# Optimization experiments

Hardware: AMD Instinct MI355X
Metric: run time of the kernel (lower is better)

Reference implementation:

```python
import jax, jax.numpy as jnp
import numpy as np

EPS = 1e-6
HEADS = 8


def _block_weights(gh, gw):
    # block centers at (i+0.5, j+0.5); 'cos' transform, column-normalized (sum over dim 0)
    ii, jj = np.meshgrid(np.arange(gh) + 0.5, np.arange(gw) + 0.5, indexing='ij')
    centers = np.stack([ii.ravel(), jj.ravel()], axis=-1)  # [N, 2]
    d = np.linalg.norm(centers[:, None, :] - centers[None, :, :], axis=-1)  # [N, N]
    mat = np.cos(d / d.max() * np.pi / 4.0)
    mat = mat / mat.sum(axis=0, keepdims=True)
    return jnp.asarray(mat, dtype=jnp.float32)


def setup_inputs() -> dict:
    key = jax.random.key(0)
    ks = jax.random.split(key, 5)
    B, N, W, C = 8, 256, 49, 512
    s = 1.0 / np.sqrt(C)
    return {
        'x': jax.random.normal(ks[0], (B, N, W, C), jnp.float32),
        'ln_g': jnp.ones((C,), jnp.float32),
        'ln_b': jnp.zeros((C,), jnp.float32),
        'w_qkv': jax.random.normal(ks[1], (3 * C, C), jnp.float32) * s,  # Linear(dim, 3*dim, bias=False)
        'lepe_w': jax.random.normal(ks[2], (C, 1, 5, 5), jnp.float32) * 0.2,  # depthwise 5x5
        'lepe_b': jnp.zeros((C,), jnp.float32),
        'w_out': jax.random.normal(ks[3], (C, C), jnp.float32) * s,
        'b_out': jnp.zeros((C,), jnp.float32),
    }


def reference(x, ln_g, ln_b, w_qkv, lepe_w, lepe_b, w_out, b_out):
    B, N, Wn, C = x.shape
    H = HEADS
    D = C // H
    gh = gw = int(round(N ** 0.5))   # grid of window blocks
    wh = ww = int(round(Wn ** 0.5))  # tokens per window side

    # LayerNorm over channel dim (torch eps=1e-5, biased var)
    mu = x.mean(-1, keepdims=True)
    var = x.var(-1, keepdims=True)
    xn = (x - mu) / jnp.sqrt(var + 1e-5) * ln_g + ln_b

    # qkv projection
    qkv = jnp.einsum('bnwc,oc->bnwo', xn, w_qkv)
    q, k, v = jnp.split(qkv, 3, axis=-1)  # each [B, N, W, C]

    # LePE: fold v to image [B, C, gh*wh, gw*ww], depthwise conv 5x5 pad 2, unfold back
    img = v.reshape(B, gh, gw, wh, ww, C).transpose(0, 5, 1, 3, 2, 4).reshape(B, C, gh * wh, gw * ww)
    lepe = jax.lax.conv_general_dilated(
        img, lepe_w, window_strides=(1, 1), padding=((2, 2), (2, 2)),
        dimension_numbers=('NCHW', 'OIHW', 'NCHW'), feature_group_count=C)
    lepe = lepe + lepe_b[None, :, None, None]
    lepe = lepe.reshape(B, C, gh, wh, gw, ww).transpose(0, 2, 4, 3, 5, 1).reshape(B, N, Wn, C)

    # ReLU + eps feature maps (qk_norm=False -> identity norms)
    q = jax.nn.relu(q) + EPS
    k = jax.nn.relu(k) + EPS

    # split heads: [B, H, N, W, D]
    def split_heads(t):
        return t.reshape(B, N, Wn, H, D).transpose(0, 3, 1, 2, 4)
    q, k, v = split_heads(q), split_heads(k), split_heads(v)

    # per-block k^T v state: [B, H, N, D, D]
    kv = jnp.einsum('bhnwd,bhnwe->bhnde', k, v)
    weight = _block_weights(gh, gw)  # [N, N]
    kv = jnp.einsum('ij,bhjde->bhide', weight, kv)

    k_sum = k.sum(axis=-2)  # [B, H, N, D]
    qk_sum = jnp.einsum('bhnwd,bhnd->bhnw', q, k_sum)[..., None]  # [B, H, N, W, 1]
    normalizer = jnp.einsum('ij,bhjwo->bhiwo', weight, qk_sum) + EPS

    out = jnp.einsum('bhnwd,bhnde->bhnwe', q, kv) / normalizer  # [B, H, N, W, D]
    out = out.transpose(0, 2, 3, 1, 4).reshape(B, N, Wn, C)
    out = out + lepe
    return jnp.einsum('bnwc,oc->bnwo', out, w_out) + b_out
```

## Files before the change

kernel.cpp:

```cpp
#include <hip/hip_runtime.h>
#include <cstdint>

typedef unsigned short u16;
typedef unsigned int   u32;
typedef u16   u16x8 __attribute__((ext_vector_type(8)));
typedef u16   u16x4 __attribute__((ext_vector_type(4)));
typedef float f32x4 __attribute__((ext_vector_type(4)));
typedef __bf16 bf16x8 __attribute__((ext_vector_type(8)));

#define NB    256
#define WTOK  49
#define CH    512
#define HEADS 8
#define DH    64
#define TOK   100352
#define CO    1536

__device__ __forceinline__ u16 f2bf(float f) {
  u32 u = __float_as_uint(f);
  u = (u + 0x7FFFu + ((u >> 16) & 1u)) >> 16;
  return (u16)u;
}
__device__ __forceinline__ float bf2f(u16 u) { return __uint_as_float(((u32)u) << 16); }

__device__ __forceinline__ void load_lds16(const void* g, void* l) {
  __builtin_amdgcn_global_load_lds(
      reinterpret_cast<__attribute__((address_space(1))) void*>(reinterpret_cast<uintptr_t>(g)),
      reinterpret_cast<__attribute__((address_space(3))) void*>(reinterpret_cast<uintptr_t>(l)),
      16, 0, 0);
}

__global__ void cvt_f32_bf16(const float* __restrict__ in, u16* __restrict__ out, int n8) {
  int i = blockIdx.x * 256 + threadIdx.x;
  if (i < n8) {
    f32x4 a = *(const f32x4*)(in + (long)i * 8);
    f32x4 b = *(const f32x4*)(in + (long)i * 8 + 4);
    u16x8 o;
    o[0]=f2bf(a[0]); o[1]=f2bf(a[1]); o[2]=f2bf(a[2]); o[3]=f2bf(a[3]);
    o[4]=f2bf(b[0]); o[5]=f2bf(b[1]); o[6]=f2bf(b[2]); o[7]=f2bf(b[3]);
    *(u16x8*)(out + (long)i * 8) = o;
  }
}

__global__ void prep_wle(const float* __restrict__ lepe_w, float* __restrict__ wle) {
  int i = blockIdx.x * 256 + threadIdx.x;
  if (i < 12800) {
    int c = i / 25, kk = i % 25;
    wle[kk * 512 + c] = lepe_w[i];
  }
}

__global__ void weight_kernel(u16* __restrict__ Wbf, float* __restrict__ Wt) {
  int j = blockIdx.x, i = threadIdx.x;
  float iy = (float)(i >> 4) + 0.5f, ix = (float)(i & 15) + 0.5f;
  float jy = (float)(j >> 4) + 0.5f, jx = (float)(j & 15) + 0.5f;
  float dy = iy - jy, dx = ix - jx;
  float d = sqrtf(dy * dy + dx * dx);
  const float dmax = 21.213203435596427f;
  float m = cosf(d * (0.78539816339744831f / dmax));
  __shared__ float red[256];
  red[i] = m;
  __syncthreads();
  for (int s = 128; s > 0; s >>= 1) {
    if (i < s) red[i] += red[i + s];
    __syncthreads();
  }
  float w = m / red[0];
  Wbf[i * 256 + j] = f2bf(w);
  Wt[j * 256 + i] = w;
}

__global__ __launch_bounds__(256) void ln_kernel(const float* __restrict__ x,
                                                 const float* __restrict__ g,
                                                 const float* __restrict__ bta,
                                                 u16* __restrict__ xn) {
  int wave = threadIdx.x >> 6, lane = threadIdx.x & 63;
  long t = (long)blockIdx.x * 4 + wave;
  const float* xp = x + t * CH + lane * 8;
  f32x4 a = *(const f32x4*)xp;
  f32x4 b = *(const f32x4*)(xp + 4);
  float s  = a[0]+a[1]+a[2]+a[3]+b[0]+b[1]+b[2]+b[3];
  float sq = a[0]*a[0]+a[1]*a[1]+a[2]*a[2]+a[3]*a[3]+b[0]*b[0]+b[1]*b[1]+b[2]*b[2]+b[3]*b[3];
  for (int m = 1; m < 64; m <<= 1) { s += __shfl_xor(s, m); sq += __shfl_xor(sq, m); }
  float mu = s * (1.0f / 512.0f);
  float var = sq * (1.0f / 512.0f) - mu * mu;
  float rstd = rsqrtf(var + 1e-5f);
  const float* gp = g + lane * 8;
  const float* bp = bta + lane * 8;
  f32x4 g0 = *(const f32x4*)gp, g1 = *(const f32x4*)(gp + 4);
  f32x4 b0 = *(const f32x4*)bp, b1 = *(const f32x4*)(bp + 4);
  u16x8 o;
  o[0] = f2bf((a[0]-mu)*rstd*g0[0] + b0[0]);
  o[1] = f2bf((a[1]-mu)*rstd*g0[1] + b0[1]);
  o[2] = f2bf((a[2]-mu)*rstd*g0[2] + b0[2]);
  o[3] = f2bf((a[3]-mu)*rstd*g0[3] + b0[3]);
  o[4] = f2bf((b[0]-mu)*rstd*g1[0] + b1[0]);
  o[5] = f2bf((b[1]-mu)*rstd*g1[1] + b1[1]);
  o[6] = f2bf((b[2]-mu)*rstd*g1[2] + b1[2]);
  o[7] = f2bf((b[3]-mu)*rstd*g1[3] + b1[3]);
  *(u16x8*)(xn + t * CH + lane * 8) = o;
}

template <int KT>
__device__ __forceinline__ void kstep8(char* sm, const u16* sA, const u16* sB,
                                       int t, int lane_off, int wm, int wn,
                                       f32x4 (&acc)[8][4]) {
  const char* base = sm + (KT & 3) * 32768 + lane_off;
  char* wbp = sm + ((KT + 3) & 3) * 32768 + t * 16;
  if constexpr (KT + 3 < 16) {
    load_lds16(sA + (KT + 3) * 32, wbp);
    load_lds16(sA + (KT + 3) * 32 + 65536, wbp + 8192);
  }
  bf16x8 bfr[4], afr[4];
#pragma unroll
  for (int n = 0; n < 4; n++) bfr[n] = *(const bf16x8*)(base + 16384 + wn * 4096 + n * 1024);
#pragma unroll
  for (int m = 0; m < 4; m++) afr[m] = *(const bf16x8*)(base + wm * 8192 + m * 1024);
  __builtin_amdgcn_s_barrier();
  __builtin_amdgcn_s_setprio(1);
#pragma unroll
  for (int m = 0; m < 4; m++)
#pragma unroll
    for (int n = 0; n < 4; n++)
      acc[m][n] = __builtin_amdgcn_mfma_f32_16x16x32_bf16(afr[m], bfr[n], acc[m][n], 0, 0, 0);
  __builtin_amdgcn_s_setprio(0);
  __builtin_amdgcn_s_barrier();
  if constexpr (KT + 3 < 16) {
    load_lds16(sB + (KT + 3) * 32, wbp + 16384);
    load_lds16(sB + (KT + 3) * 32 + 65536, wbp + 24576);
  }
#pragma unroll
  for (int m = 0; m < 4; m++) afr[m] = *(const bf16x8*)(base + wm * 8192 + (4 + m) * 1024);
  __builtin_amdgcn_s_barrier();
  __builtin_amdgcn_s_setprio(1);
#pragma unroll
  for (int m = 0; m < 4; m++)
#pragma unroll
    for (int n = 0; n < 4; n++)
      acc[4 + m][n] = __builtin_amdgcn_mfma_f32_16x16x32_bf16(afr[m], bfr[n], acc[4 + m][n], 0, 0, 0);
  __builtin_amdgcn_s_setprio(0);
  if constexpr (KT < 13) {
    asm volatile("s_waitcnt vmcnt(8)" ::: "memory");
  } else if constexpr (KT == 13) {
    asm volatile("s_waitcnt vmcnt(4)" ::: "memory");
  } else if constexpr (KT == 14) {
    asm volatile("s_waitcnt vmcnt(0)" ::: "memory");
  }
  if constexpr (KT < 15) __builtin_amdgcn_s_barrier();
}

template <int EPI>
__global__ __launch_bounds__(512, 2)
void gemm8(const u16* __restrict__ A, const u16* __restrict__ B,
           void* __restrict__ C, const float* __restrict__ bias, int N, int nbn) {
  __shared__ __align__(16) char sm[131072];
  const int nwg = gridDim.x;
  const int bid = blockIdx.x;
  const int cpx = nwg >> 3;
  const int vid = (bid & 7) * cpx + (bid >> 3);
  const int bn = vid % nbn, bm = vid / nbn;
  const int t = threadIdx.x;
  const int lane = t & 63, wave = t >> 6;
  const int wm = wave >> 2, wn = wave & 3;
  const int fr = lane & 15, fq = lane >> 4;
  const int lane_off = (fr >> 1) * 128 + ((((fr & 1) << 2) + fq) ^ (fr >> 1)) * 16;
  const int sl = (t & 7) ^ ((t >> 3) & 7);
  const u16* sA = A + ((long)bm * 256 + ((t >> 3) << 1) + (sl >> 2)) * 512 + (sl & 3) * 8;
  const u16* sB = B + ((long)bn * 256 + ((t >> 3) << 1) + (sl >> 2)) * 512 + (sl & 3) * 8;
  f32x4 acc[8][4] = {};
#pragma unroll
  for (int kt = 0; kt < 3; kt++) {
    char* d = sm + kt * 32768 + t * 16;
    load_lds16(sA + kt * 32, d);
    load_lds16(sA + kt * 32 + 65536, d + 8192);
    load_lds16(sB + kt * 32, d + 16384);
    load_lds16(sB + kt * 32 + 65536, d + 24576);
  }
  asm volatile("s_waitcnt vmcnt(8)" ::: "memory");
  __builtin_amdgcn_s_barrier();
  kstep8<0>(sm, sA, sB, t, lane_off, wm, wn, acc);
  kstep8<1>(sm, sA, sB, t, lane_off, wm, wn, acc);
  kstep8<2>(sm, sA, sB, t, lane_off, wm, wn, acc);
  kstep8<3>(sm, sA, sB, t, lane_off, wm, wn, acc);
  kstep8<4>(sm, sA, sB, t, lane_off, wm, wn, acc);
  kstep8<5>(sm, sA, sB, t, lane_off, wm, wn, acc);
  kstep8<6>(sm, sA, sB, t, lane_off, wm, wn, acc);
  kstep8<7>(sm, sA, sB, t, lane_off, wm, wn, acc);
  kstep8<8>(sm, sA, sB, t, lane_off, wm, wn, acc);
  kstep8<9>(sm, sA, sB, t, lane_off, wm, wn, acc);
  kstep8<10>(sm, sA, sB, t, lane_off, wm, wn, acc);
  kstep8<11>(sm, sA, sB, t, lane_off, wm, wn, acc);
  kstep8<12>(sm, sA, sB, t, lane_off, wm, wn, acc);
  kstep8<13>(sm, sA, sB, t, lane_off, wm, wn, acc);
  kstep8<14>(sm, sA, sB, t, lane_off, wm, wn, acc);
  kstep8<15>(sm, sA, sB, t, lane_off, wm, wn, acc);
  const long r0 = (long)bm * 256 + wm * 128 + fq * 4;
  const int c0 = bn * 256 + wn * 64 + fr;
#pragma unroll
  for (int m = 0; m < 8; m++) {
#pragma unroll
    for (int n = 0; n < 4; n++) {
      int c = c0 + n * 16;
#pragma unroll
      for (int jj = 0; jj < 4; jj++) {
        long r = r0 + m * 16 + jj;
        float v = acc[m][n][jj];
        if (EPI == 1) {
          if (c < 1024) v = fmaxf(v, 0.0f) + 1e-6f;
          ((u16*)C)[r * N + c] = f2bf(v);
        } else if (EPI == 2) {
          ((float*)C)[r * N + c] = v + bias[c];
        } else {
          ((u16*)C)[r * N + c] = f2bf(v);
        }
      }
    }
  }
}

template <int EPI>
__global__ __launch_bounds__(256)
void gemm_bt(const u16* __restrict__ A, const u16* __restrict__ B,
             void* __restrict__ C, const float* __restrict__ bias,
             int M, int N, int K, long sAb, long sBb, long sCb) {
  __shared__ u16 As[128 * 32];
  __shared__ u16 Bs[128 * 32];
  const int tid = threadIdx.x;
  const int lane = tid & 63;
  const int wave = tid >> 6;
  const int fr = lane & 15, fq = lane >> 4;
  const int wr = (wave >> 1) * 64, wc = (wave & 1) * 64;
  const long bm = blockIdx.y, bn = blockIdx.x, bz = blockIdx.z;
  const u16* Ab = A + bz * sAb + bm * 128 * (long)K;
  const u16* Bb = B + bz * sBb + bn * 128 * (long)K;
  const int srow = tid >> 2;
  const int scol = (tid & 3) * 8;
  f32x4 acc[4][4] = {};
  for (int k0 = 0; k0 < K; k0 += 32) {
    load_lds16(Ab + (long)srow * K + k0 + scol, As + tid * 8);
    load_lds16(Ab + (long)(srow + 64) * K + k0 + scol, As + 2048 + tid * 8);
    load_lds16(Bb + (long)srow * K + k0 + scol, Bs + tid * 8);
    load_lds16(Bb + (long)(srow + 64) * K + k0 + scol, Bs + 2048 + tid * 8);
    __syncthreads();
    bf16x8 af[4], bf[4];
#pragma unroll
    for (int m = 0; m < 4; m++) af[m] = *(const bf16x8*)&As[(wr + m * 16 + fr) * 32 + fq * 8];
#pragma unroll
    for (int n = 0; n < 4; n++) bf[n] = *(const bf16x8*)&Bs[(wc + n * 16 + fr) * 32 + fq * 8];
#pragma unroll
    for (int m = 0; m < 4; m++)
#pragma unroll
      for (int n = 0; n < 4; n++)
        acc[m][n] = __builtin_amdgcn_mfma_f32_16x16x32_bf16(af[m], bf[n], acc[m][n], 0, 0, 0);
    __syncthreads();
  }
#pragma unroll
  for (int m = 0; m < 4; m++) {
    int r0 = wr + m * 16 + fq * 4;
#pragma unroll
    for (int n = 0; n < 4; n++) {
      int c = (int)bn * 128 + wc + n * 16 + fr;
#pragma unroll
      for (int jj = 0; jj < 4; jj++) {
        long r = bm * 128 + r0 + jj;
        float v = acc[m][n][jj];
        if (EPI == 1) { if (c < 1024) v = fmaxf(v, 0.0f) + 1e-6f; }
        if (EPI == 2) {
          ((float*)C)[bz * sCb + r * N + c] = v + bias[c];
        } else {
          ((u16*)C)[bz * sCb + r * N + c] = f2bf(v);
        }
      }
    }
  }
}

__global__ __launch_bounds__(256)
void fold_v(const u16* __restrict__ qkv, u16* __restrict__ vimg) {
  long i = (long)blockIdx.x * 256 + threadIdx.x;
  int tok = (int)(i >> 6);
  int c0 = ((int)i & 63) * 8;
  int w = tok % WTOK, n = tok / WTOK;
  int b = n >> 8, blk = n & 255;
  int gi = blk >> 4, gj = blk & 15;
  int wi = w / 7, wj = w - wi * 7;
  int y = gi * 7 + wi + 2, x = gj * 7 + wj + 2;
  u16x8 v = *(const u16x8*)(qkv + (long)tok * CO + 1024 + c0);
  *(u16x8*)(vimg + (((long)(b * 116 + y)) * 116 + x) * 512 + c0) = v;
}

__global__ __launch_bounds__(256)
void zero_border(u16* __restrict__ vimg) {
  int y = blockIdx.x, b = blockIdx.y;
  int tid = threadIdx.x;
  u16* row = vimg + ((long)(b * 116 + y)) * 116 * 512;
  u16x8 z = {};
  if (y < 2 || y >= 114) {
    for (int i = tid; i < 116 * 512 / 8; i += 256) *(u16x8*)(row + i * 8) = z;
  } else {
    int col = tid >> 6;
    int x = (col < 2) ? col : 112 + col;
    *(u16x8*)(row + x * 512 + (tid & 63) * 8) = z;
  }
}

__global__ __launch_bounds__(256, 2)
void lepe_conv3(const u16* __restrict__ vimg, const float* __restrict__ wle,
                const float* __restrict__ lb, u16* __restrict__ lepe) {
  const int tid = threadIdx.x;
  const int c0 = (tid & 127) * 4;
  const int x  = blockIdx.x * 2 + (tid >> 7);
  const int ys = blockIdx.y * 14;
  const int b  = blockIdx.z;
  f32x4 wv[25];
#pragma unroll
  for (int k = 0; k < 25; k++) wv[k] = *(const f32x4*)(wle + k * 512 + c0);
  const f32x4 bias = *(const f32x4*)(lb + c0);
  const u16* rbase = vimg + (((long)(b * 116 + ys)) * 116 + x) * 512 + c0;
  u16x4 win[5][5];
#pragma unroll
  for (int j = 0; j < 4; j++) {
    const u16* rp = rbase + (long)j * (116 * 512);
#pragma unroll
    for (int kx = 0; kx < 5; kx++) win[j][kx] = *(const u16x4*)(rp + kx * 512);
  }
  const int gj = x / 7, wj = x - gj * 7;
  u16* ob = lepe + (((long)(b * 256 + blockIdx.y * 32 + gj)) * 49 + wj) * 512 + c0;
#pragma unroll
  for (int i = 0; i < 14; i++) {
    {
      const u16* rp = rbase + (long)(i + 4) * (116 * 512);
#pragma unroll
      for (int kx = 0; kx < 5; kx++) win[(i + 4) % 5][kx] = *(const u16x4*)(rp + kx * 512);
    }
    f32x4 acc = bias;
#pragma unroll
    for (int s = 0; s < 5; s++)
#pragma unroll
      for (int kx = 0; kx < 5; kx++) {
        u16x4 v = win[(i + s) % 5][kx];
        f32x4 w = wv[s * 5 + kx];
#pragma unroll
        for (int c = 0; c < 4; c++) acc[c] += bf2f(v[c]) * w[c];
      }
    u16x4 o;
#pragma unroll
    for (int c = 0; c < 4; c++) o[c] = f2bf(acc[c]);
    *(u16x4*)(ob + ((i / 7) * 784 + (i % 7) * 7) * 512) = o;
  }
}

__global__ __launch_bounds__(256)
void kv_local_kernel(const u16* __restrict__ qkv, u16* __restrict__ KVl,
                     float* __restrict__ qk_sum) {
  int n = blockIdx.x, h = blockIdx.y, b = blockIdx.z;
  int bh = b * HEADS + h;
  long tbase = ((long)(b * NB + n)) * WTOK;
  __shared__ u16 kT[64 * 72];
  __shared__ u16 vT[64 * 72];
  __shared__ u16 qs[49 * 72];
  __shared__ float ksum[64];
  __shared__ float qkp[256];
  int tid = threadIdx.x;
  for (int i = tid; i < (64 * 72) / 2; i += 256) {
    ((u32*)kT)[i] = 0;
    ((u32*)vT)[i] = 0;
  }
  __syncthreads();
  {
    int w = tid >> 3, d0 = (tid & 7) * 8;
    u16x8 k8 = *(const u16x8*)(qkv + (tbase + w) * CO + 512 + h * 64 + d0);
    u16x8 v8 = *(const u16x8*)(qkv + (tbase + w) * CO + 1024 + h * 64 + d0);
#pragma unroll
    for (int i = 0; i < 8; i++) { kT[(d0 + i) * 72 + w] = k8[i]; vT[(d0 + i) * 72 + w] = v8[i]; }
    int w2 = w + 32;
    if (w2 < WTOK) {
      u16x8 k82 = *(const u16x8*)(qkv + (tbase + w2) * CO + 512 + h * 64 + d0);
      u16x8 v82 = *(const u16x8*)(qkv + (tbase + w2) * CO + 1024 + h * 64 + d0);
#pragma unroll
      for (int i = 0; i < 8; i++) { kT[(d0 + i) * 72 + w2] = k82[i]; vT[(d0 + i) * 72 + w2] = v82[i]; }
    }
    if (tid < 196) {
      int wq = tid >> 2, dq = (tid & 3) * 16;
      u16x8 q0 = *(const u16x8*)(qkv + (tbase + wq) * CO + h * 64 + dq);
      u16x8 q1 = *(const u16x8*)(qkv + (tbase + wq) * CO + h * 64 + dq + 8);
      *(u16x8*)&qs[wq * 72 + dq] = q0;
      *(u16x8*)&qs[wq * 72 + dq + 8] = q1;
    }
  }
  __syncthreads();
  if (tid < 64) {
    float s = 0.0f;
#pragma unroll
    for (int c = 0; c < 9; c++) {
      u16x8 r = *(const u16x8*)&kT[tid * 72 + c * 8];
#pragma unroll
      for (int i = 0; i < 8; i++) s += bf2f(r[i]);
    }
    ksum[tid] = s;
  }
  __syncthreads();
  if (tid < 196) {
    int w = tid >> 2, d0 = (tid & 3) * 16;
    float s = 0.0f;
#pragma unroll
    for (int i = 0; i < 16; i++) s += bf2f(qs[w * 72 + d0 + i]) * ksum[d0 + i];
    qkp[tid] = s;
  }
  __syncthreads();
  if (tid < WTOK) {
    float s = qkp[tid * 4] + qkp[tid * 4 + 1] + qkp[tid * 4 + 2] + qkp[tid * 4 + 3];
    qk_sum[((long)bh * NB + n) * WTOK + tid] = s;
  }
  int lane = tid & 63, wave = tid >> 6;
  int fr = lane & 15, fq = lane >> 4;
  f32x4 acc[4] = {};
#pragma unroll
  for (int ks = 0; ks < 2; ks++) {
    bf16x8 a = *(const bf16x8*)&kT[(wave * 16 + fr) * 72 + ks * 32 + fq * 8];
#pragma unroll
    for (int n4 = 0; n4 < 4; n4++) {
      bf16x8 bb = *(const bf16x8*)&vT[(n4 * 16 + fr) * 72 + ks * 32 + fq * 8];
      acc[n4] = __builtin_amdgcn_mfma_f32_16x16x32_bf16(a, bb, acc[n4], 0, 0, 0);
    }
  }
  long obase = ((long)bh * NB + n) * 4096;
#pragma unroll
  for (int n4 = 0; n4 < 4; n4++)
#pragma unroll
    for (int jj = 0; jj < 4; jj++) {
      int d = wave * 16 + fq * 4 + jj;
      int e = n4 * 16 + fr;
      KVl[obase + d * 64 + e] = f2bf(acc[n4][jj]);
    }
}

__global__ __launch_bounds__(256)
void transpose_kv(const u16* __restrict__ in, u16* __restrict__ out) {
  int dt = blockIdx.x, jt = blockIdx.y, bh = blockIdx.z;
  __shared__ u16 t[64 * 72];
  int tid = threadIdx.x;
  {
    int jr = tid >> 2, c0 = (tid & 3) * 16;
    const u16* ip = in + ((long)bh * NB + jt * 64 + jr) * 4096 + dt * 64 + c0;
    *(u16x8*)&t[jr * 72 + c0] = *(const u16x8*)ip;
    *(u16x8*)&t[jr * 72 + c0 + 8] = *(const u16x8*)(ip + 8);
  }
  __syncthreads();
  {
    int der = tid >> 2, j0 = (tid & 3) * 16;
    u16x8 o0, o1;
#pragma unroll
    for (int i = 0; i < 8; i++) o0[i] = t[(j0 + i) * 72 + der];
#pragma unroll
    for (int i = 0; i < 8; i++) o1[i] = t[(j0 + 8 + i) * 72 + der];
    u16* op = out + ((long)bh * 4096 + dt * 64 + der) * 256 + jt * 64 + j0;
    *(u16x8*)op = o0;
    *(u16x8*)(op + 8) = o1;
  }
}

__global__ __launch_bounds__(256)
void norm_kernel(const float* __restrict__ Wt, const float* __restrict__ qk_sum,
                 float* __restrict__ inv_norm) {
  int bh = blockIdx.x, tid = threadIdx.x;
  __shared__ float qk[NB * WTOK];
  for (int i = tid; i < NB * WTOK; i += 256) qk[i] = qk_sum[(long)bh * NB * WTOK + i];
  __syncthreads();
  float acc[WTOK];
#pragma unroll
  for (int w = 0; w < WTOK; w++) acc[w] = 0.0f;
  for (int j = 0; j < NB; j++) {
    float wv = Wt[j * NB + tid];
#pragma unroll
    for (int w = 0; w < WTOK; w++) acc[w] += wv * qk[j * WTOK + w];
  }
  long ob = ((long)bh * NB + tid) * WTOK;
#pragma unroll
  for (int w = 0; w < WTOK; w++) inv_norm[ob + w] = 1.0f / (acc[w] + 1e-6f);
}

__global__ __launch_bounds__(256)
void attn_out_kernel(const u16* __restrict__ qkv, const u16* __restrict__ kvm,
                     const float* __restrict__ inv_norm, const u16* __restrict__ lepe,
                     u16* __restrict__ ebuf) {
  int n = blockIdx.x, h = blockIdx.y, b = blockIdx.z;
  int bh = b * HEADS + h;
  long tbase = ((long)(b * NB + n)) * WTOK;
  __shared__ u16 qs[64 * 72];
  __shared__ u16 kvT[64 * 72];
  __shared__ float inv[WTOK];
  int tid = threadIdx.x;
  if (tid < 196) {
    int w = tid >> 2, d0 = (tid & 3) * 16;
    u16x8 q0 = *(const u16x8*)(qkv + (tbase + w) * CO + h * 64 + d0);
    u16x8 q1 = *(const u16x8*)(qkv + (tbase + w) * CO + h * 64 + d0 + 8);
    *(u16x8*)&qs[w * 72 + d0] = q0;
    *(u16x8*)&qs[w * 72 + d0 + 8] = q1;
  }
  {
    int d = tid >> 2, e0 = (tid & 3) * 16;
    const u16* kp = kvm + ((long)bh * NB + n) * 4096 + d * 64 + e0;
    u16x8 k0 = *(const u16x8*)kp;
    u16x8 k1 = *(const u16x8*)(kp + 8);
#pragma unroll
    for (int i = 0; i < 8; i++) { kvT[(e0 + i) * 72 + d] = k0[i]; kvT[(e0 + 8 + i) * 72 + d] = k1[i]; }
  }
  if (tid < WTOK) inv[tid] = inv_norm[((long)bh * NB + n) * WTOK + tid];
  __syncthreads();
  int lane = tid & 63, wave = tid >> 6;
  int fr = lane & 15, fq = lane >> 4;
  f32x4 acc[4] = {};
#pragma unroll
  for (int ks = 0; ks < 2; ks++) {
    bf16x8 a = *(const bf16x8*)&qs[(wave * 16 + fr) * 72 + ks * 32 + fq * 8];
#pragma unroll
    for (int n4 = 0; n4 < 4; n4++) {
      bf16x8 bb = *(const bf16x8*)&kvT[(n4 * 16 + fr) * 72 + ks * 32 + fq * 8];
      acc[n4] = __builtin_amdgcn_mfma_f32_16x16x32_bf16(a, bb, acc[n4], 0, 0, 0);
    }
  }
#pragma unroll
  for (int n4 = 0; n4 < 4; n4++)
#pragma unroll
    for (int jj = 0; jj < 4; jj++) {
      int w = wave * 16 + fq * 4 + jj;
      if (w < WTOK) {
        int e = n4 * 16 + fr;
        long off = (tbase + w) * CH + h * 64 + e;
        float v = acc[n4][jj] * inv[w] + bf2f(lepe[off]);
        ebuf[off] = f2bf(v);
      }
    }
}

static const size_t OFF_XN    = 0;
static const size_t OFF_QKV   = 102760448;
static const size_t OFF_KVL   = OFF_QKV + 308281344;
static const size_t OFF_KVT   = OFF_KVL + 134217728;
static const size_t OFF_QKS   = OFF_KVT + 134217728;
static const size_t OFF_INV   = OFF_QKS + 3211264;
static const size_t OFF_WBF   = OFF_INV + 3211264;
static const size_t OFF_WTF   = OFF_WBF + 131072;
static const size_t OFF_WQKVB = OFF_WTF + 262144;
static const size_t OFF_WOUTB = OFF_WQKVB + 1572864;
static const size_t OFF_WLE   = OFF_WOUTB + 524288;

extern "C" void kernel_launch(void* const* d_in, const int* in_sizes, int n_in,
                              void* d_out, int out_size, void* d_ws, size_t ws_size,
                              hipStream_t stream) {
  const float* x      = (const float*)d_in[0];
  const float* ln_g   = (const float*)d_in[1];
  const float* ln_b   = (const float*)d_in[2];
  const float* w_qkv  = (const float*)d_in[3];
  const float* lepe_w = (const float*)d_in[4];
  const float* lepe_b = (const float*)d_in[5];
  const float* w_out  = (const float*)d_in[6];
  const float* b_out  = (const float*)d_in[7];
  float* out = (float*)d_out;
  char* ws = (char*)d_ws;

  u16*   xn     = (u16*)(ws + OFF_XN);
  u16*   lepe   = (u16*)(ws + OFF_XN);
  u16*   qkv    = (u16*)(ws + OFF_QKV);
  u16*   KVl    = (u16*)(ws + OFF_KVL);
  u16*   kvm    = (u16*)(ws + OFF_KVL);
  u16*   vimg   = (u16*)(ws + OFF_KVT);
  u16*   KVT    = (u16*)(ws + OFF_KVT);
  u16*   ebuf   = (u16*)(ws + OFF_KVT);
  float* qks    = (float*)(ws + OFF_QKS);
  float* invn   = (float*)(ws + OFF_INV);
  u16*   Wbf    = (u16*)(ws + OFF_WBF);
  float* Wt     = (float*)(ws + OFF_WTF);
  u16*   wqkvb  = (u16*)(ws + OFF_WQKVB);
  u16*   woutb  = (u16*)(ws + OFF_WOUTB);
  float* wle    = (float*)(ws + OFF_WLE);

  cvt_f32_bf16<<<384, 256, 0, stream>>>(w_qkv, wqkvb, 98304);
  cvt_f32_bf16<<<128, 256, 0, stream>>>(w_out, woutb, 32768);
  prep_wle<<<50, 256, 0, stream>>>(lepe_w, wle);
  weight_kernel<<<256, 256, 0, stream>>>(Wbf, Wt);
  zero_border<<<dim3(116, 8), 256, 0, stream>>>(vimg);

  ln_kernel<<<25088, 256, 0, stream>>>(x, ln_g, ln_b, xn);

  gemm8<1><<<2352, 512, 0, stream>>>(xn, wqkvb, (void*)qkv, nullptr, CO, 6);

  fold_v<<<25088, 256, 0, stream>>>(qkv, vimg);
  lepe_conv3<<<dim3(56, 8, 8), 256, 0, stream>>>(vimg, wle, lepe_b, lepe);

  kv_local_kernel<<<dim3(NB, HEADS, 8), 256, 0, stream>>>(qkv, KVl, qks);

  transpose_kv<<<dim3(64, 4, 64), 256, 0, stream>>>(KVl, KVT);

  gemm_bt<0><<<dim3(32, 2, 64), 256, 0, stream>>>(Wbf, KVT, (void*)kvm, nullptr,
                                                  NB, 4096, NB,
                                                  0, (long)4096 * 256, (long)256 * 4096);

  norm_kernel<<<64, 256, 0, stream>>>(Wt, qks, invn);

  attn_out_kernel<<<dim3(NB, HEADS, 8), 256, 0, stream>>>(qkv, kvm, invn, lepe, ebuf);

  gemm8<2><<<784, 512, 0, stream>>>(ebuf, woutb, (void*)out, b_out, CH, 2);
}
```

Measured before the change: 898.8 us.

## Register double-buffer GEMM fragments and deepen LDS prefetch to four stages

```diff
diff --git a/kernel.cpp b/kernel.cpp
--- a/kernel.cpp
+++ b/kernel.cpp
@@ -102,51 +102,42 @@
 }
 
 template <int KT>
-__device__ __forceinline__ void kstep8(char* sm, const u16* sA, const u16* sB,
+__device__ __forceinline__ void kstep9(char* sm, const u16* sA, const u16* sB,
                                        int t, int lane_off, int wm, int wn,
-                                       f32x4 (&acc)[8][4]) {
-  const char* base = sm + (KT & 3) * 32768 + lane_off;
-  char* wbp = sm + ((KT + 3) & 3) * 32768 + t * 16;
-  if constexpr (KT + 3 < 16) {
-    load_lds16(sA + (KT + 3) * 32, wbp);
-    load_lds16(sA + (KT + 3) * 32 + 65536, wbp + 8192);
-  }
-  bf16x8 bfr[4], afr[4];
-#pragma unroll
-  for (int n = 0; n < 4; n++) bfr[n] = *(const bf16x8*)(base + 16384 + wn * 4096 + n * 1024);
-#pragma unroll
-  for (int m = 0; m < 4; m++) afr[m] = *(const bf16x8*)(base + wm * 8192 + m * 1024);
-  __builtin_amdgcn_s_barrier();
+                                       f32x4 (&acc)[8][4], bf16x8 (&fa)[2][8], bf16x8 (&fb)[2][4]) {
+  constexpr int cur = KT & 1, nxt = cur ^ 1;
+  if constexpr (KT + 4 < 16) {
+    char* wbp = sm + ((KT + 4) & 3) * 32768 + t * 16;
+    load_lds16(sA + (KT + 4) * 32, wbp);
+    load_lds16(sA + (KT + 4) * 32 + 65536, wbp + 8192);
+    load_lds16(sB + (KT + 4) * 32, wbp + 16384);
+    load_lds16(sB + (KT + 4) * 32 + 65536, wbp + 24576);
+  }
+  if constexpr (KT + 1 < 16) {
+    const char* base = sm + ((KT + 1) & 3) * 32768 + lane_off;
+#pragma unroll
+    for (int n = 0; n < 4; n++) fb[nxt][n] = *(const bf16x8*)(base + 16384 + wn * 4096 + n * 1024);
+#pragma unroll
+    for (int m = 0; m < 8; m++) fa[nxt][m] = *(const bf16x8*)(base + wm * 8192 + m * 1024);
+  }
   __builtin_amdgcn_s_setprio(1);
 #pragma unroll
-  for (int m = 0; m < 4; m++)
+  for (int m = 0; m < 8; m++)
 #pragma unroll
     for (int n = 0; n < 4; n++)
-      acc[m][n] = __builtin_amdgcn_mfma_f32_16x16x32_bf16(afr[m], bfr[n], acc[m][n], 0, 0, 0);
+      acc[m][n] = __builtin_amdgcn_mfma_f32_16x16x32_bf16(fa[cur][m], fb[cur][n], acc[m][n], 0, 0, 0);
   __builtin_amdgcn_s_setprio(0);
-  __builtin_amdgcn_s_barrier();
-  if constexpr (KT + 3 < 16) {
-    load_lds16(sB + (KT + 3) * 32, wbp + 16384);
-    load_lds16(sB + (KT + 3) * 32 + 65536, wbp + 24576);
-  }
-#pragma unroll
-  for (int m = 0; m < 4; m++) afr[m] = *(const bf16x8*)(base + wm * 8192 + (4 + m) * 1024);
-  __builtin_amdgcn_s_barrier();
-  __builtin_amdgcn_s_setprio(1);
-#pragma unroll
-  for (int m = 0; m < 4; m++)
-#pragma unroll
-    for (int n = 0; n < 4; n++)
-      acc[4 + m][n] = __builtin_amdgcn_mfma_f32_16x16x32_bf16(afr[m], bfr[n], acc[4 + m][n], 0, 0, 0);
-  __builtin_amdgcn_s_setprio(0);
-  if constexpr (KT < 13) {
+  if constexpr (KT < 14) {
+    asm volatile("s_waitcnt lgkmcnt(0)" ::: "memory");
+  }
+  if constexpr (KT + 4 < 16) {
     asm volatile("s_waitcnt vmcnt(8)" ::: "memory");
+  } else if constexpr (KT == 12) {
+    asm volatile("s_waitcnt vmcnt(4)" ::: "memory");
   } else if constexpr (KT == 13) {
-    asm volatile("s_waitcnt vmcnt(4)" ::: "memory");
-  } else if constexpr (KT == 14) {
     asm volatile("s_waitcnt vmcnt(0)" ::: "memory");
   }
-  if constexpr (KT < 15) __builtin_amdgcn_s_barrier();
+  if constexpr (KT < 14) __builtin_amdgcn_s_barrier();
 }
 
 template <int EPI>
@@ -168,8 +159,9 @@
   const u16* sA = A + ((long)bm * 256 + ((t >> 3) << 1) + (sl >> 2)) * 512 + (sl & 3) * 8;
   const u16* sB = B + ((long)bn * 256 + ((t >> 3) << 1) + (sl >> 2)) * 512 + (sl & 3) * 8;
   f32x4 acc[8][4] = {};
-#pragma unroll
-  for (int kt = 0; kt < 3; kt++) {
+  bf16x8 fa[2][8], fb[2][4];
+#pragma unroll
+  for (int kt = 0; kt < 4; kt++) {
     char* d = sm + kt * 32768 + t * 16;
     load_lds16(sA + kt * 32, d);
     load_lds16(sA + kt * 32 + 65536, d + 8192);
@@ -178,22 +170,31 @@
   }
   asm volatile("s_waitcnt vmcnt(8)" ::: "memory");
   __builtin_amdgcn_s_barrier();
-  kstep8<0>(sm, sA, sB, t, lane_off, wm, wn, acc);
-  kstep8<1>(sm, sA, sB, t, lane_off, wm, wn, acc);
-  kstep8<2>(sm, sA, sB, t, lane_off, wm, wn, acc);
-  kstep8<3>(sm, sA, sB, t, lane_off, wm, wn, acc);
-  kstep8<4>(sm, sA, sB, t, lane_off, wm, wn, acc);
-  kstep8<5>(sm, sA, sB, t, lane_off, wm, wn, acc);
-  kstep8<6>(sm, sA, sB, t, lane_off, wm, wn, acc);
-  kstep8<7>(sm, sA, sB, t, lane_off, wm, wn, acc);
-  kstep8<8>(sm, sA, sB, t, lane_off, wm, wn, acc);
-  kstep8<9>(sm, sA, sB, t, lane_off, wm, wn, acc);
-  kstep8<10>(sm, sA, sB, t, lane_off, wm, wn, acc);
-  kstep8<11>(sm, sA, sB, t, lane_off, wm, wn, acc);
-  kstep8<12>(sm, sA, sB, t, lane_off, wm, wn, acc);
-  kstep8<13>(sm, sA, sB, t, lane_off, wm, wn, acc);
-  kstep8<14>(sm, sA, sB, t, lane_off, wm, wn, acc);
-  kstep8<15>(sm, sA, sB, t, lane_off, wm, wn, acc);
+  {
+    const char* base = sm + lane_off;
+#pragma unroll
+    for (int n = 0; n < 4; n++) fb[0][n] = *(const bf16x8*)(base + 16384 + wn * 4096 + n * 1024);
+#pragma unroll
+    for (int m = 0; m < 8; m++) fa[0][m] = *(const bf16x8*)(base + wm * 8192 + m * 1024);
+  }
+  asm volatile("s_waitcnt lgkmcnt(0)" ::: "memory");
+  __builtin_amdgcn_s_barrier();
+  kstep9<0>(sm, sA, sB, t, lane_off, wm, wn, acc, fa, fb);
+  kstep9<1>(sm, sA, sB, t, lane_off, wm, wn, acc, fa, fb);
+  kstep9<2>(sm, sA, sB, t, lane_off, wm, wn, acc, fa, fb);
+  kstep9<3>(sm, sA, sB, t, lane_off, wm, wn, acc, fa, fb);
+  kstep9<4>(sm, sA, sB, t, lane_off, wm, wn, acc, fa, fb);
+  kstep9<5>(sm, sA, sB, t, lane_off, wm, wn, acc, fa, fb);
+  kstep9<6>(sm, sA, sB, t, lane_off, wm, wn, acc, fa, fb);
+  kstep9<7>(sm, sA, sB, t, lane_off, wm, wn, acc, fa, fb);
+  kstep9<8>(sm, sA, sB, t, lane_off, wm, wn, acc, fa, fb);
+  kstep9<9>(sm, sA, sB, t, lane_off, wm, wn, acc, fa, fb);
+  kstep9<10>(sm, sA, sB, t, lane_off, wm, wn, acc, fa, fb);
+  kstep9<11>(sm, sA, sB, t, lane_off, wm, wn, acc, fa, fb);
+  kstep9<12>(sm, sA, sB, t, lane_off, wm, wn, acc, fa, fb);
+  kstep9<13>(sm, sA, sB, t, lane_off, wm, wn, acc, fa, fb);
+  kstep9<14>(sm, sA, sB, t, lane_off, wm, wn, acc, fa, fb);
+  kstep9<15>(sm, sA, sB, t, lane_off, wm, wn, acc, fa, fb);
   const long r0 = (long)bm * 256 + wm * 128 + fq * 4;
   const int c0 = bn * 256 + wn * 64 + fr;
 #pragma unroll
```

Result: no change. 906.8 us (+0.9%).
